# Optimization experiments

Hardware: AMD Instinct MI355X
Metric: run time of the kernel (lower is better)

The kernel has to match this reference:

```python
import jax, jax.numpy as jnp
from jax import lax
import numpy as np

H = W = 768
N_BOXES = 512
C1, C2 = 32, 64
POOL = 5
NUM_CLASSES = 4
BN_EPS = 1e-5


def setup_inputs() -> dict:
    key = jax.random.key(0)
    ks = jax.random.split(key, 20)
    image = jax.random.normal(ks[0], (1, 3, H, W), jnp.float32)
    # valid boxes: xmax>xmin, ymax>ymin, inside [0, W)
    xmin = jax.random.randint(ks[1], (N_BOXES,), 0, W - 256)
    ymin = jax.random.randint(ks[2], (N_BOXES,), 0, H - 256)
    bw = jax.random.randint(ks[3], (N_BOXES,), 8, 256)
    bh = jax.random.randint(ks[4], (N_BOXES,), 8, 256)
    boxes = jnp.stack([xmin, ymin, xmin + bw, ymin + bh], axis=1).astype(jnp.int32)
    conv1_w = jax.random.normal(ks[5], (C1, 3, 3, 3), jnp.float32) * 0.1
    conv1_b = jax.random.normal(ks[6], (C1,), jnp.float32) * 0.01
    bn1_g = 1.0 + 0.1 * jax.random.normal(ks[7], (C1,), jnp.float32)
    bn1_b = 0.1 * jax.random.normal(ks[8], (C1,), jnp.float32)
    bn1_m = 0.1 * jax.random.normal(ks[9], (C1,), jnp.float32)
    bn1_v = jax.random.uniform(ks[10], (C1,), jnp.float32, 0.5, 1.5)
    conv2_w = jax.random.normal(ks[11], (C2, C1, 3, 3), jnp.float32) * 0.05
    conv2_b = jax.random.normal(ks[12], (C2,), jnp.float32) * 0.01
    bn2_g = 1.0 + 0.1 * jax.random.normal(ks[13], (C2,), jnp.float32)
    bn2_b = 0.1 * jax.random.normal(ks[14], (C2,), jnp.float32)
    bn2_m = 0.1 * jax.random.normal(ks[15], (C2,), jnp.float32)
    bn2_v = jax.random.uniform(ks[16], (C2,), jnp.float32, 0.5, 1.5)
    fc1_w = jax.random.normal(ks[17], (128, C2 * POOL * POOL), jnp.float32) * 0.02
    fc1_b = jnp.zeros((128,), jnp.float32)
    fc2_w = jax.random.normal(ks[18], (NUM_CLASSES, 128), jnp.float32) * 0.05
    fc2_b = jnp.zeros((NUM_CLASSES,), jnp.float32)
    return dict(image=image, boxes=boxes,
                conv1_w=conv1_w, conv1_b=conv1_b, bn1_g=bn1_g, bn1_b=bn1_b, bn1_m=bn1_m, bn1_v=bn1_v,
                conv2_w=conv2_w, conv2_b=conv2_b, bn2_g=bn2_g, bn2_b=bn2_b, bn2_m=bn2_m, bn2_v=bn2_v,
                fc1_w=fc1_w, fc1_b=fc1_b, fc2_w=fc2_w, fc2_b=fc2_b)


def _conv(x, w, b):
    y = lax.conv_general_dilated(x, w, (1, 1), ((1, 1), (1, 1)),
                                 dimension_numbers=("NCHW", "OIHW", "NCHW"))
    return y + b[None, :, None, None]


def _bn(x, g, b, m, v):
    scale = g / jnp.sqrt(v + BN_EPS)
    return x * scale[None, :, None, None] + (b - m * scale)[None, :, None, None]


def _forward(image, boxes, conv1_w, conv1_b, bn1_g, bn1_b, bn1_m, bn1_v,
             conv2_w, conv2_b, bn2_g, bn2_b, bn2_m, bn2_v,
             fc1_w, fc1_b, fc2_w, fc2_b):
    # backbone: Conv -> ReLU -> BN (order as in source), twice
    x = _bn(jax.nn.relu(_conv(image, conv1_w, conv1_b)), bn1_g, bn1_b, bn1_m, bn1_v)
    x = _bn(jax.nn.relu(_conv(x, conv2_w, conv2_b)), bn2_g, bn2_b, bn2_m, bn2_v)
    feat = x[0]  # [C2, H, W], batch assumed 1 as in the per-box slicing loop
    # integral image for exact adaptive-avg-pool over integer index rectangles
    integ = jnp.pad(feat, ((0, 0), (1, 0), (1, 0))).cumsum(1).cumsum(2)  # [C2,H+1,W+1]
    xmin, ymin, xmax, ymax = boxes[:, 0], boxes[:, 1], boxes[:, 2], boxes[:, 3]
    bh = ymax - ymin
    bw = xmax - xmin
    i = jnp.arange(POOL)
    # AdaptiveAvgPool2d bin edges: start=floor(i*L/5), end=ceil((i+1)*L/5)
    y0 = ymin[:, None] + (i * bh[:, None]) // POOL            # [N,5]
    y1 = ymin[:, None] + ((i + 1) * bh[:, None] + POOL - 1) // POOL
    x0 = xmin[:, None] + (i * bw[:, None]) // POOL
    x1 = xmin[:, None] + ((i + 1) * bw[:, None] + POOL - 1) // POOL

    def rect(ys, xs):  # [C2, N, 5, 5]
        return integ[:, ys[:, :, None], xs[:, None, :]]

    s = rect(y1, x1) - rect(y0, x1) - rect(y1, x0) + rect(y0, x0)
    area = ((y1 - y0)[:, :, None] * (x1 - x0)[:, None, :]).astype(feat.dtype)  # [N,5,5]
    pooled = s / area[None]                                    # [C2,N,5,5]
    flat = pooled.transpose(1, 0, 2, 3).reshape(boxes.shape[0], -1)  # [N, C2*25]
    h1 = jax.nn.relu(flat @ fc1_w.T + fc1_b)  # dropout is identity in eval
    return h1 @ fc2_w.T + fc2_b               # [N, num_classes]


def reference(image, boxes, conv1_w, conv1_b, bn1_g, bn1_b, bn1_m, bn1_v,
              conv2_w, conv2_b, bn2_g, bn2_b, bn2_m, bn2_v,
              fc1_w, fc1_b, fc2_w, fc2_b):
    return _forward(image, boxes, conv1_w, conv1_b, bn1_g, bn1_b, bn1_m, bn1_v,
                    conv2_w, conv2_b, bn2_g, bn2_b, bn2_m, bn2_v,
                    fc1_w, fc1_b, fc2_w, fc2_b)
```

## Files before the change

### kernel.cpp

```cpp
#include <hip/hip_runtime.h>
#include <hip/hip_bf16.h>

#define HH 768
#define WW 768
#define HWSZ (HH*WW)
#define BN_EPS 1e-5f
#define SEG 8
#define NSEG 96

typedef __attribute__((ext_vector_type(8))) short bf16x8;
typedef __attribute__((ext_vector_type(4))) float f32x4;

__device__ __forceinline__ float bf2f(unsigned short u) {
  union { unsigned int i; float f; } v; v.i = ((unsigned int)u) << 16; return v.f;
}
__device__ __forceinline__ unsigned short f2bf(float f) {
  union { float f; unsigned int i; } v; v.f = f;
  unsigned int x = v.i;
  return (unsigned short)((x + 0x7fffu + ((x >> 16) & 1u)) >> 16);
}
__device__ __forceinline__ float ldf(const void* p, int i, int flag) {
  return flag ? bf2f(((const unsigned short*)p)[i]) : ((const float*)p)[i];
}

#define DPP_ADD(v, CTRL) do {                                              \
    union { float f; int i; } _u; _u.f = (v);                              \
    int _t = __builtin_amdgcn_update_dpp(0, _u.i, (CTRL), 0xf, 0xf, true); \
    union { int i; float f; } _w; _w.i = _t;                               \
    (v) += _w.f;                                                           \
  } while (0)
__device__ __forceinline__ float row_prefix16(float v) {
  DPP_ADD(v, 0x111);
  DPP_ADD(v, 0x112);
  DPP_ADD(v, 0x114);
  DPP_ADD(v, 0x118);
  return v;
}

__device__ __forceinline__ int detect_flag(const void* v1) {
  const unsigned short* v1raw = (const unsigned short*)v1;
  int ok = 1;
  #pragma unroll
  for (int j = 0; j < 4; ++j) {
    unsigned short u = v1raw[2*j];
    if (u < 0x3E00u || u > 0x4040u) ok = 0;
  }
  return ok;
}

__global__ void k_prep(const void* __restrict__ c1b,
                       const void* __restrict__ g1, const void* __restrict__ b1,
                       const void* __restrict__ m1, const void* __restrict__ v1,
                       const void* __restrict__ c2b, const void* __restrict__ g2,
                       const void* __restrict__ b2, const void* __restrict__ m2,
                       const void* __restrict__ v2, const void* __restrict__ w1,
                       const void* __restrict__ fb1, const void* __restrict__ fw2,
                       const void* __restrict__ fb2, const void* __restrict__ w2,
                       const void* __restrict__ fw1,
                       int* __restrict__ flagp, float* __restrict__ cst,
                       unsigned short* __restrict__ A2, unsigned short* __restrict__ A1,
                       unsigned short* __restrict__ w1c)
{
  int flag = detect_flag(v1);
  int tid = threadIdx.x, bid = blockIdx.x;
  int gid = bid * 256 + tid;

  if (bid == 0) {
    if (tid == 0) *flagp = flag;
    float* bias1 = cst + 864;
    float* sc1   = cst + 896;
    float* sh1   = cst + 928;
    float* bias2 = cst + 960;
    float* sc2   = cst + 1024;
    float* sh2   = cst + 1088;
    float* fb1c  = cst + 1152;
    float* w2c   = cst + 1280;
    float* fb2c  = cst + 1792;
    if (tid < 32) {
      float s = ldf(g1, tid, flag) * rsqrtf(ldf(v1, tid, flag) + BN_EPS);
      sc1[tid] = s;
      sh1[tid] = ldf(b1, tid, flag) - ldf(m1, tid, flag) * s;
      bias1[tid] = ldf(c1b, tid, flag);
    }
    if (tid < 64) {
      float s = ldf(g2, tid, flag) * rsqrtf(ldf(v2, tid, flag) + BN_EPS);
      sc2[tid] = s;
      sh2[tid] = ldf(b2, tid, flag) - ldf(m2, tid, flag) * s;
      bias2[tid] = ldf(c2b, tid, flag);
    }
    if (tid < 128) fb1c[tid] = ldf(fb1, tid, flag);
    if (tid < 4)   fb2c[tid] = ldf(fb2, tid, flag);
    for (int i = tid; i < 512; i += 256) w2c[i] = ldf(fw2, i, flag);
  }
  if (gid < 80*288) {
    int o = gid / 288, k = gid % 288, tap = k >> 5, ci = k & 31;
    A2[gid] = (o < 64) ? f2bf(ldf(w2, (o*32 + ci)*9 + tap, flag)) : (unsigned short)0;
  }
  if (gid < 32*64) {
    int o = gid >> 6, k = gid & 63, tap = k >> 2, ci = k & 3;
    A1[gid] = (tap < 9 && ci < 3) ? f2bf(ldf(w1, o*27 + ci*9 + tap, flag))
                                  : (unsigned short)0;
  }
  for (int i = gid; i < 128*1600; i += 128*256) {
    int t = i / 1600, r = i % 1600, cell = r >> 6, c = r & 63;
    w1c[i] = f2bf(ldf(fw1, t*1600 + c*25 + cell, flag));
  }
}

__global__ __launch_bounds__(256) void k_conv1m(const void* __restrict__ img,
    const int* __restrict__ flagp, const unsigned short* __restrict__ A1,
    const float* __restrict__ cst, unsigned short* __restrict__ feat1)
{
  const float* bias1 = cst + 864;
  const float* sc1   = cst + 896;
  const float* sh1   = cst + 928;
  int flag = *flagp;
  __shared__ unsigned short tile[18 * 34 * 4];
  int tid = threadIdx.x;
  int x0 = blockIdx.x * 32, ybase = blockIdx.y * 16;

  for (int idx = tid; idx < 18*34; idx += 256) {
    int r = idx / 34, p = idx % 34;
    int gy = ybase - 1 + r, gx = x0 - 1 + p;
    unsigned short e0 = 0, e1 = 0, e2 = 0;
    if (gy >= 0 && gy < HH && gx >= 0 && gx < WW) {
      e0 = f2bf(ldf(img, 0*HWSZ + gy*WW + gx, flag));
      e1 = f2bf(ldf(img, 1*HWSZ + gy*WW + gx, flag));
      e2 = f2bf(ldf(img, 2*HWSZ + gy*WW + gx, flag));
    }
    ushort4 pk; pk.x = e0; pk.y = e1; pk.z = e2; pk.w = 0;
    *(ushort4*)(tile + idx*4) = pk;
  }

  int w = tid >> 6, lane = tid & 63, quad = lane >> 4, l16 = lane & 15;
  bf16x8 a1f[2][2];
  #pragma unroll
  for (int mt = 0; mt < 2; ++mt)
    #pragma unroll
    for (int kt = 0; kt < 2; ++kt)
      a1f[mt][kt] = *(const bf16x8*)(A1 + (mt*16 + l16)*64 + kt*32 + quad*8);
  int t0 = 2*quad, t1 = 2*quad + 1;
  int ky0 = t0/3, kx0 = t0%3, ky1 = t1/3, kx1 = t1%3;
  __syncthreads();

  for (int dyw = 0; dyw < 4; ++dyw) {
    int dy = dyw*4 + w;
    int y = ybase + dy;
    f32x4 acc[2][2];
    #pragma unroll
    for (int mt = 0; mt < 2; ++mt)
      #pragma unroll
      for (int i = 0; i < 2; ++i)
        acc[mt][i] = (f32x4){0.f,0.f,0.f,0.f};
    #pragma unroll
    for (int i = 0; i < 2; ++i) {
      int pxb = i*16 + l16;
      union { uint2 u[2]; bf16x8 v; } b0;
      b0.u[0] = *(const uint2*)(tile + ((dy + ky0)*34 + pxb + kx0)*4);
      b0.u[1] = *(const uint2*)(tile + ((dy + ky1)*34 + pxb + kx1)*4);
      union { uint2 u[2]; bf16x8 v; } b1v;
      b1v.u[0] = *(const uint2*)(tile + ((dy + 2)*34 + pxb + 2)*4);
      b1v.u[1] = make_uint2(0u, 0u);
      #pragma unroll
      for (int mt = 0; mt < 2; ++mt) {
        acc[mt][i] = __builtin_amdgcn_mfma_f32_16x16x32_bf16(a1f[mt][0], b0.v, acc[mt][i], 0, 0, 0);
        acc[mt][i] = __builtin_amdgcn_mfma_f32_16x16x32_bf16(a1f[mt][1], b1v.v, acc[mt][i], 0, 0, 0);
      }
    }
    #pragma unroll
    for (int mt = 0; mt < 2; ++mt) {
      int cb = mt*16 + quad*4;
      float bs0 = bias1[cb], bs1 = bias1[cb+1], bs2 = bias1[cb+2], bs3 = bias1[cb+3];
      float s0 = sc1[cb], s1 = sc1[cb+1], s2 = sc1[cb+2], s3 = sc1[cb+3];
      float h0 = sh1[cb], h1 = sh1[cb+1], h2 = sh1[cb+2], h3 = sh1[cb+3];
      #pragma unroll
      for (int i = 0; i < 2; ++i) {
        int px = x0 + i*16 + l16;
        ushort4 pk;
        pk.x = f2bf(fmaxf(acc[mt][i][0] + bs0, 0.f) * s0 + h0);
        pk.y = f2bf(fmaxf(acc[mt][i][1] + bs1, 0.f) * s1 + h1);
        pk.z = f2bf(fmaxf(acc[mt][i][2] + bs2, 0.f) * s2 + h2);
        pk.w = f2bf(fmaxf(acc[mt][i][3] + bs3, 0.f) * s3 + h3);
        *(ushort4*)(feat1 + ((size_t)(y*WW + px))*32 + cb) = pk;
      }
    }
  }
}

__global__ __launch_bounds__(256) void k_conv2t(const unsigned short* __restrict__ feat1,
    const unsigned short* __restrict__ A2, const float* __restrict__ cst,
    float* __restrict__ T)
{
  const float* bias2 = cst + 960;
  const float* sc2   = cst + 1024;
  const float* sh2   = cst + 1088;
  __shared__ unsigned short tile[10 * 34 * 40];
  int tid = threadIdx.x;
  int xb = blockIdx.x, ys = blockIdx.y;
  int x0 = xb * 32, ybase = ys * SEG;

  for (int idx = tid; idx < 10*34*4; idx += 256) {
    int q = idx & 3, p = (idx >> 2) % 34, r = idx / 136;
    int gy = ybase - 1 + r, gx = x0 - 1 + p;
    uint4 val = make_uint4(0u, 0u, 0u, 0u);
    if (gy >= 0 && gy < HH && gx >= 0 && gx < WW)
      val = *(const uint4*)(feat1 + (gy*WW + gx)*32 + q*8);
    *(uint4*)(tile + (r*34 + p)*40 + q*8) = val;
  }

  int w = tid >> 6, lane = tid & 63, quad = lane >> 4, l16 = lane & 15;
  int m = w * 16 + l16;
  bf16x8 afrag[9];
  #pragma unroll
  for (int t = 0; t < 9; ++t)
    afrag[t] = *(const bf16x8*)(A2 + m*288 + t*32 + quad*8);
  float bs[4], scv[4], shv[4];
  #pragma unroll
  for (int r = 0; r < 4; ++r) {
    int c = w*16 + quad*4 + r;
    bs[r] = bias2[c]; scv[r] = sc2[c]; shv[r] = sh2[c];
  }
  __syncthreads();

  f32x4 ys0 = (f32x4){0.f,0.f,0.f,0.f};
  f32x4 ys1 = (f32x4){0.f,0.f,0.f,0.f};
  int cbase = w*16 + quad*4;
  for (int dy = 0; dy < SEG; ++dy) {
    int y = ybase + dy;
    f32x4 acc[2];
    acc[0] = (f32x4){0.f,0.f,0.f,0.f};
    acc[1] = (f32x4){0.f,0.f,0.f,0.f};
    #pragma unroll
    for (int t = 0; t < 9; ++t) {
      int ky = t / 3, kx = t % 3;
      #pragma unroll
      for (int i = 0; i < 2; ++i) {
        int px = i*16 + l16 + kx;
        bf16x8 b = *(const bf16x8*)(tile + ((dy + ky)*34 + px)*40 + quad*8);
        acc[i] = __builtin_amdgcn_mfma_f32_16x16x32_bf16(afrag[t], b, acc[i], 0, 0, 0);
      }
    }
    #pragma unroll
    for (int r = 0; r < 4; ++r) {
      float v0 = fmaxf(acc[0][r] + bs[r], 0.f) * scv[r] + shv[r];
      float v1 = fmaxf(acc[1][r] + bs[r], 0.f) * scv[r] + shv[r];
      v0 = row_prefix16(v0);
      v1 = row_prefix16(v1);
      v1 += __shfl(v0, 15, 16);
      ys0[r] += v0;
      ys1[r] += v1;
    }
    *(f32x4*)(T + ((size_t)(y*WW + x0 + l16))*64 + cbase)      = ys0;
    *(f32x4*)(T + ((size_t)(y*WW + x0 + 16 + l16))*64 + cbase) = ys1;
  }
}

__global__ __launch_bounds__(256) void k_cgen(const float* __restrict__ T,
                                              float* __restrict__ C)
{
  __shared__ float Sp[NSEG*24];
  int cc = blockIdx.x, tid = threadIdx.x;
  for (int idx = tid; idx < NSEG*24; idx += 256) {
    int i = idx / 24, j = idx % 24;
    Sp[idx] = T[((size_t)((i*SEG + SEG-1)*WW + j*32 + 31))*64 + cc];
  }
  __syncthreads();
  if (tid < 24) {
    float run = 0.f;
    for (int i = 0; i < NSEG; ++i) { run += Sp[i*24 + tid]; Sp[i*24 + tid] = run; }
  }
  __syncthreads();
  if (tid < NSEG) {
    float run = 0.f;
    #pragma unroll
    for (int j = 0; j < 24; ++j) { run += Sp[tid*24 + j]; Sp[tid*24 + j] = run; }
  }
  __syncthreads();
  for (int idx = tid; idx < NSEG*24; idx += 256)
    C[((size_t)idx)*64 + cc] = Sp[idx];
}

__global__ __launch_bounds__(256) void k_ab(const float* __restrict__ T,
    const float* __restrict__ C, float* __restrict__ A, float* __restrict__ Bp)
{
  int part = blockIdx.y, tid = threadIdx.x;
  int c = tid & 63, s = tid >> 6;
  if (part == 0) {
    int y = blockIdx.x * 4 + s;
    float run = 0.f;
    #pragma unroll
    for (int j = 0; j < 24; ++j) {
      run += T[((size_t)(y*WW + j*32 + 31))*64 + c];
      A[((size_t)(y*24 + j))*64 + c] = run;
    }
  } else {
    int x = blockIdx.x * 4 + s;
    int j = x >> 5;
    float run = 0.f;
    #pragma unroll 4
    for (int i = 0; i < NSEG; ++i) {
      run += T[((size_t)((i*SEG + SEG-1)*WW + x))*64 + c];
      float cj = (j > 0) ? C[((size_t)(i*24 + (j-1)))*64 + c] : 0.f;
      Bp[((size_t)(i*WW + x))*64 + c] = run + cj;
    }
  }
}

__device__ __forceinline__ float icorner(const float* __restrict__ T,
    const float* __restrict__ A, const float* __restrict__ Bp,
    int c, int yy, int xx)
{
  int i = yy >> 3, j = xx >> 5;
  float v = T[((size_t)(yy*WW + xx))*64 + c];
  if (j > 0) v += A[((size_t)(yy*24 + (j-1)))*64 + c];
  if (i > 0) v += Bp[((size_t)((i-1)*WW + xx))*64 + c];
  return v;
}

__global__ __launch_bounds__(256) void k_roi3(const float* __restrict__ T,
    const float* __restrict__ A, const float* __restrict__ Bp,
    const int* __restrict__ boxes, unsigned short* __restrict__ flat)
{
  int b = blockIdx.x;
  int xmin = boxes[b*4 + 0], ymin = boxes[b*4 + 1];
  int xmax = boxes[b*4 + 2], ymax = boxes[b*4 + 3];
  int bh = ymax - ymin, bw = xmax - xmin;
  for (int idx = threadIdx.x; idx < 1600; idx += 256) {
    int c = idx & 63, cell = idx >> 6, i = cell / 5, j = cell % 5;
    int y0 = ymin + (i*bh)/5,  y1 = ymin + ((i+1)*bh + 4)/5;
    int x0 = xmin + (j*bw)/5,  x1 = xmin + ((j+1)*bw + 4)/5;
    float s = icorner(T, A, Bp, c, y1-1, x1-1);
    if (y0 > 0)           s -= icorner(T, A, Bp, c, y0-1, x1-1);
    if (x0 > 0)           s -= icorner(T, A, Bp, c, y1-1, x0-1);
    if (y0 > 0 && x0 > 0) s += icorner(T, A, Bp, c, y0-1, x0-1);
    float area = (float)((y1 - y0) * (x1 - x0));
    flat[b*1600 + cell*64 + c] = f2bf(s / area);
  }
}

__global__ __launch_bounds__(256) void k_fcm(const unsigned short* __restrict__ flat,
    const unsigned short* __restrict__ w1c, const float* __restrict__ cst,
    const int* __restrict__ flagp, void* __restrict__ out)
{
  const float* fb1c = cst + 1152;
  const float* w2c  = cst + 1280;
  const float* fb2c = cst + 1792;
  __shared__ unsigned short sflat[16 * 1608];
  __shared__ float hbuf[16 * 132];
  int tid = threadIdx.x;
  int b0 = blockIdx.x * 16;
  for (int ii = tid; ii < 3200; ii += 256) {
    int bi = ii / 200, ch = ii % 200;
    *(uint4*)(sflat + bi*1608 + ch*8) = *(const uint4*)(flat + (b0 + bi)*1600 + ch*8);
  }
  __syncthreads();
  int w = tid >> 6, lane = tid & 63, quad = lane >> 4, l16 = lane & 15;
  f32x4 acc[2];
  acc[0] = (f32x4){0.f,0.f,0.f,0.f};
  acc[1] = (f32x4){0.f,0.f,0.f,0.f};
  for (int kt = 0; kt < 50; ++kt) {
    bf16x8 b = *(const bf16x8*)(sflat + l16*1608 + kt*32 + quad*8);
    #pragma unroll
    for (int mt = 0; mt < 2; ++mt) {
      bf16x8 a = *(const bf16x8*)(w1c + ((w*2 + mt)*16 + l16)*1600 + kt*32 + quad*8);
      acc[mt] = __builtin_amdgcn_mfma_f32_16x16x32_bf16(a, b, acc[mt], 0, 0, 0);
    }
  }
  #pragma unroll
  for (int mt = 0; mt < 2; ++mt) {
    #pragma unroll
    for (int r = 0; r < 4; ++r) {
      int h = (w*2 + mt)*16 + quad*4 + r;
      hbuf[l16*132 + h] = fmaxf(acc[mt][r] + fb1c[h], 0.f);
    }
  }
  __syncthreads();
  if (tid < 64) {
    int bi = tid >> 2, o = tid & 3;
    float a2 = fb2c[o];
    for (int k = 0; k < 128; ++k) a2 += hbuf[bi*132 + k] * w2c[o*128 + k];
    if (*flagp) ((unsigned short*)out)[(b0 + bi)*4 + o] = f2bf(a2);
    else        ((float*)out)[(b0 + bi)*4 + o] = a2;
  }
}

__global__ __launch_bounds__(256) void k_conv2_c16(const unsigned short* __restrict__ feat1,
    const unsigned short* __restrict__ A2, const float* __restrict__ cst,
    float* __restrict__ chunk, int c0, int cnw)
{
  const float* bias2 = cst + 960;
  const float* sc2   = cst + 1024;
  const float* sh2   = cst + 1088;
  __shared__ unsigned short tile[3 * 130 * 40];
  int tid = threadIdx.x;
  int y = blockIdx.y, x0 = blockIdx.x * 128;
  for (int idx = tid; idx < 3*130*4; idx += 256) {
    int q = idx & 3, p = (idx >> 2) % 130, r = idx / 520;
    int gy = y - 1 + r, gx = x0 - 1 + p;
    uint4 val = make_uint4(0u, 0u, 0u, 0u);
    if (gy >= 0 && gy < HH && gx >= 0 && gx < WW)
      val = *(const uint4*)(feat1 + (gy*WW + gx)*32 + q*8);
    *(uint4*)(tile + (r*130 + p)*40 + q*8) = val;
  }
  __syncthreads();
  int w = tid >> 6, lane = tid & 63, quad = lane >> 4, l16 = lane & 15;
  int m = c0 + l16;
  f32x4 acc[2];
  acc[0] = (f32x4){0.f,0.f,0.f,0.f};
  acc[1] = (f32x4){0.f,0.f,0.f,0.f};
  #pragma unroll
  for (int t = 0; t < 9; ++t) {
    int ky = t / 3, kx = t % 3;
    bf16x8 a = *(const bf16x8*)(A2 + m*288 + t*32 + quad*8);
    #pragma unroll
    for (int i = 0; i < 2; ++i) {
      int px = w*32 + i*16 + l16 + kx;
      bf16x8 b = *(const bf16x8*)(tile + (ky*130 + px)*40 + quad*8);
      acc[i] = __builtin_amdgcn_mfma_f32_16x16x32_bf16(a, b, acc[i], 0, 0, 0);
    }
  }
  #pragma unroll
  for (int r = 0; r < 4; ++r) {
    int cl = quad*4 + r;
    if (cl < cnw) {
      int c = c0 + cl;
      float bsv = bias2[c], s = sc2[c], sh = sh2[c];
      float* dst = chunk + cl*HWSZ + y*WW;
      #pragma unroll
      for (int i = 0; i < 2; ++i) {
        float v = fmaxf(acc[i][r] + bsv, 0.f) * s + sh;
        dst[x0 + w*32 + i*16 + l16] = v;
      }
    }
  }
}
__global__ __launch_bounds__(256) void k_csy(float* __restrict__ buf) {
  int t = blockIdx.x * 256 + threadIdx.x;
  int c = t / WW, x = t % WW;
  float* p = buf + c*HWSZ + x;
  float run = 0.f;
  for (int yb = 0; yb < HH; yb += 16) {
    float v[16];
    #pragma unroll
    for (int j = 0; j < 16; ++j) v[j] = p[(yb + j) * WW];
    #pragma unroll
    for (int j = 0; j < 16; ++j) { run += v[j]; v[j] = run; }
    #pragma unroll
    for (int j = 0; j < 16; ++j) p[(yb + j) * WW] = v[j];
  }
}
__global__ __launch_bounds__(256) void k_csx(float* __restrict__ buf) {
  int row = blockIdx.x * 4 + (threadIdx.x >> 6);
  int lane = threadIdx.x & 63;
  float* p = buf + (long)row * WW;
  float carry = 0.f;
  for (int ch = 0; ch < 12; ++ch) {
    float v = p[ch*64 + lane];
    #pragma unroll
    for (int off = 1; off < 64; off <<= 1) {
      float t = __shfl_up(v, off);
      v = (lane >= off) ? v + t : v;
    }
    v += carry;
    p[ch*64 + lane] = v;
    carry = __shfl(v, 63);
  }
}
__global__ __launch_bounds__(256) void k_roi(const float* __restrict__ integ,
    const int* __restrict__ boxes, unsigned short* __restrict__ flat, int c0, int cn)
{
  int b = blockIdx.x;
  int xmin = boxes[b*4 + 0], ymin = boxes[b*4 + 1];
  int xmax = boxes[b*4 + 2], ymax = boxes[b*4 + 3];
  int bh = ymax - ymin, bw = xmax - xmin;
  for (int idx = threadIdx.x; idx < cn*25; idx += 256) {
    int cl = idx / 25, cell = idx % 25, i = cell / 5, j = cell % 5;
    int y0 = ymin + (i*bh)/5,      y1 = ymin + ((i+1)*bh + 4)/5;
    int x0 = xmin + (j*bw)/5,      x1 = xmin + ((j+1)*bw + 4)/5;
    const float* I = integ + cl*HWSZ;
    float a  = I[(y1-1)*WW + (x1-1)];
    float bl = (y0 > 0) ? I[(y0-1)*WW + (x1-1)] : 0.f;
    float cr = (x0 > 0) ? I[(y1-1)*WW + (x0-1)] : 0.f;
    float d  = (y0 > 0 && x0 > 0) ? I[(y0-1)*WW + (x0-1)] : 0.f;
    float s = a - bl - cr + d;
    float area = (float)((y1 - y0) * (x1 - x0));
    flat[b*1600 + cell*64 + (c0 + cl)] = f2bf(s / area);
  }
}

extern "C" void kernel_launch(void* const* d_in, const int* in_sizes, int n_in,
                              void* d_out, int out_size, void* d_ws, size_t ws_size,
                              hipStream_t stream) {
  const void* img = d_in[0];
  const int* boxes = (const int*)d_in[1];
  const void* c1w = d_in[2];  const void* c1b = d_in[3];
  const void* g1  = d_in[4];  const void* b1  = d_in[5];
  const void* m1  = d_in[6];  const void* v1  = d_in[7];
  const void* c2w = d_in[8];  const void* c2b = d_in[9];
  const void* g2  = d_in[10]; const void* b2  = d_in[11];
  const void* m2  = d_in[12]; const void* v2  = d_in[13];
  const void* fw1 = d_in[14]; const void* fb1 = d_in[15];
  const void* fw2 = d_in[16]; const void* fb2 = d_in[17];

  char* ws = (char*)d_ws;
  unsigned short* A2 = (unsigned short*)ws;
  unsigned short* A1 = (unsigned short*)(ws + 46080);
  float* cst = (float*)(ws + 50176);
  int* flag = (int*)(ws + 57360);
  unsigned short* w1c  = (unsigned short*)(ws + 3592224);
  unsigned short* flat = (unsigned short*)(ws + 4001824);
  unsigned short* feat1 = (unsigned short*)(ws + 7278624);
  float* T = (float*)(ws + 45027360);
  float* Aarr = (float*)(ws + 7278624);
  float* Bparr = Aarr + (size_t)768*24*64;
  float* Carr = Bparr + (size_t)NSEG*768*64;

  const size_t base = 45027360;
  int cn;
  if      (ws_size >= base + 64ull*HWSZ*4) cn = 64;
  else if (ws_size >= base + 16ull*HWSZ*4) cn = 16;
  else if (ws_size >= base +  8ull*HWSZ*4) cn = 8;
  else if (ws_size >= base +  4ull*HWSZ*4) cn = 4;
  else if (ws_size >= base +  2ull*HWSZ*4) cn = 2;
  else                                     cn = 1;

  hipLaunchKernelGGL(k_prep, dim3(128), dim3(256), 0, stream,
                     c1b, g1, b1, m1, v1, c2b, g2, b2, m2, v2, c1w,
                     fb1, fw2, fb2, c2w, fw1, flag, cst, A2, A1, w1c);
  hipLaunchKernelGGL(k_conv1m, dim3(24, 48), dim3(256), 0, stream,
                     img, flag, A1, cst, feat1);

  if (cn == 64) {
    hipLaunchKernelGGL(k_conv2t, dim3(24, NSEG), dim3(256), 0, stream,
                       feat1, A2, cst, T);
    hipLaunchKernelGGL(k_cgen, dim3(64), dim3(256), 0, stream, T, Carr);
    hipLaunchKernelGGL(k_ab, dim3(192, 2), dim3(256), 0, stream, T, Carr, Aarr, Bparr);
    hipLaunchKernelGGL(k_roi3, dim3(512), dim3(256), 0, stream,
                       T, Aarr, Bparr, boxes, flat);
  } else {
    for (int c0 = 0; c0 < 64; c0 += cn) {
      hipLaunchKernelGGL(k_conv2_c16, dim3(6, 768), dim3(256), 0, stream,
                         feat1, A2, cst, T, c0, cn);
      hipLaunchKernelGGL(k_csy, dim3(cn*3), dim3(256), 0, stream, T);
      hipLaunchKernelGGL(k_csx, dim3(cn*192), dim3(256), 0, stream, T);
      hipLaunchKernelGGL(k_roi, dim3(512), dim3(256), 0, stream, T, boxes, flat, c0, cn);
    }
  }
  hipLaunchKernelGGL(k_fcm, dim3(32), dim3(256), 0, stream, flat, w1c, cst, flag,
                     d_out);
}
```

Baseline: 228.0 us.

## Fuse conv1 into conv2 tile kernel and parallelize row/column prefix scans

Conv1 is now computed per block on a 10x34 halo tile straight from the image into shared memory, and conv2 reads that tile directly. This removes the feat1 round trip through global memory and one kernel launch. The cost is recomputing conv1 on overlapping halo rows and columns, plus more shared memory per block. Separately, k_ab splits each row and column scan across four thread groups and combines partial sums through shared memory, which gives four times more blocks.

```diff
diff --git a/kernel.cpp b/kernel.cpp
--- a/kernel.cpp
+++ b/kernel.cpp
@@ -107,21 +107,27 @@
   }
 }
 
-__global__ __launch_bounds__(256) void k_conv1m(const void* __restrict__ img,
+__global__ __launch_bounds__(256) void k_conv12t(const void* __restrict__ img,
     const int* __restrict__ flagp, const unsigned short* __restrict__ A1,
-    const float* __restrict__ cst, unsigned short* __restrict__ feat1)
+    const unsigned short* __restrict__ A2, const float* __restrict__ cst,
+    float* __restrict__ T)
 {
   const float* bias1 = cst + 864;
   const float* sc1   = cst + 896;
   const float* sh1   = cst + 928;
+  const float* bias2 = cst + 960;
+  const float* sc2   = cst + 1024;
+  const float* sh2   = cst + 1088;
+  __shared__ unsigned short ftile[10 * 34 * 40];
+  __shared__ unsigned short itile[12 * 36 * 4];
   int flag = *flagp;
-  __shared__ unsigned short tile[18 * 34 * 4];
   int tid = threadIdx.x;
-  int x0 = blockIdx.x * 32, ybase = blockIdx.y * 16;
-
-  for (int idx = tid; idx < 18*34; idx += 256) {
-    int r = idx / 34, p = idx % 34;
-    int gy = ybase - 1 + r, gx = x0 - 1 + p;
+  int xb = blockIdx.x, ys = blockIdx.y;
+  int x0 = xb * 32, ybase = ys * SEG;
+
+  for (int idx = tid; idx < 12*36; idx += 256) {
+    int r = idx / 36, p = idx % 36;
+    int gy = ybase - 2 + r, gx = x0 - 2 + p;
     unsigned short e0 = 0, e1 = 0, e2 = 0;
     if (gy >= 0 && gy < HH && gx >= 0 && gx < WW) {
       e0 = f2bf(ldf(img, 0*HWSZ + gy*WW + gx, flag));
@@ -129,10 +135,11 @@
       e2 = f2bf(ldf(img, 2*HWSZ + gy*WW + gx, flag));
     }
     ushort4 pk; pk.x = e0; pk.y = e1; pk.z = e2; pk.w = 0;
-    *(ushort4*)(tile + idx*4) = pk;
+    *(ushort4*)(itile + idx*4) = pk;
   }
 
   int w = tid >> 6, lane = tid & 63, quad = lane >> 4, l16 = lane & 15;
+
   bf16x8 a1f[2][2];
   #pragma unroll
   for (int mt = 0; mt < 2; ++mt)
@@ -141,74 +148,7 @@
       a1f[mt][kt] = *(const bf16x8*)(A1 + (mt*16 + l16)*64 + kt*32 + quad*8);
   int t0 = 2*quad, t1 = 2*quad + 1;
   int ky0 = t0/3, kx0 = t0%3, ky1 = t1/3, kx1 = t1%3;
-  __syncthreads();
-
-  for (int dyw = 0; dyw < 4; ++dyw) {
-    int dy = dyw*4 + w;
-    int y = ybase + dy;
-    f32x4 acc[2][2];
-    #pragma unroll
-    for (int mt = 0; mt < 2; ++mt)
-      #pragma unroll
-      for (int i = 0; i < 2; ++i)
-        acc[mt][i] = (f32x4){0.f,0.f,0.f,0.f};
-    #pragma unroll
-    for (int i = 0; i < 2; ++i) {
-      int pxb = i*16 + l16;
-      union { uint2 u[2]; bf16x8 v; } b0;
-      b0.u[0] = *(const uint2*)(tile + ((dy + ky0)*34 + pxb + kx0)*4);
-      b0.u[1] = *(const uint2*)(tile + ((dy + ky1)*34 + pxb + kx1)*4);
-      union { uint2 u[2]; bf16x8 v; } b1v;
-      b1v.u[0] = *(const uint2*)(tile + ((dy + 2)*34 + pxb + 2)*4);
-      b1v.u[1] = make_uint2(0u, 0u);
-      #pragma unroll
-      for (int mt = 0; mt < 2; ++mt) {
-        acc[mt][i] = __builtin_amdgcn_mfma_f32_16x16x32_bf16(a1f[mt][0], b0.v, acc[mt][i], 0, 0, 0);
-        acc[mt][i] = __builtin_amdgcn_mfma_f32_16x16x32_bf16(a1f[mt][1], b1v.v, acc[mt][i], 0, 0, 0);
-      }
-    }
-    #pragma unroll
-    for (int mt = 0; mt < 2; ++mt) {
-      int cb = mt*16 + quad*4;
-      float bs0 = bias1[cb], bs1 = bias1[cb+1], bs2 = bias1[cb+2], bs3 = bias1[cb+3];
-      float s0 = sc1[cb], s1 = sc1[cb+1], s2 = sc1[cb+2], s3 = sc1[cb+3];
-      float h0 = sh1[cb], h1 = sh1[cb+1], h2 = sh1[cb+2], h3 = sh1[cb+3];
-      #pragma unroll
-      for (int i = 0; i < 2; ++i) {
-        int px = x0 + i*16 + l16;
-        ushort4 pk;
-        pk.x = f2bf(fmaxf(acc[mt][i][0] + bs0, 0.f) * s0 + h0);
-        pk.y = f2bf(fmaxf(acc[mt][i][1] + bs1, 0.f) * s1 + h1);
-        pk.z = f2bf(fmaxf(acc[mt][i][2] + bs2, 0.f) * s2 + h2);
-        pk.w = f2bf(fmaxf(acc[mt][i][3] + bs3, 0.f) * s3 + h3);
-        *(ushort4*)(feat1 + ((size_t)(y*WW + px))*32 + cb) = pk;
-      }
-    }
-  }
-}
-
-__global__ __launch_bounds__(256) void k_conv2t(const unsigned short* __restrict__ feat1,
-    const unsigned short* __restrict__ A2, const float* __restrict__ cst,
-    float* __restrict__ T)
-{
-  const float* bias2 = cst + 960;
-  const float* sc2   = cst + 1024;
-  const float* sh2   = cst + 1088;
-  __shared__ unsigned short tile[10 * 34 * 40];
-  int tid = threadIdx.x;
-  int xb = blockIdx.x, ys = blockIdx.y;
-  int x0 = xb * 32, ybase = ys * SEG;
-
-  for (int idx = tid; idx < 10*34*4; idx += 256) {
-    int q = idx & 3, p = (idx >> 2) % 34, r = idx / 136;
-    int gy = ybase - 1 + r, gx = x0 - 1 + p;
-    uint4 val = make_uint4(0u, 0u, 0u, 0u);
-    if (gy >= 0 && gy < HH && gx >= 0 && gx < WW)
-      val = *(const uint4*)(feat1 + (gy*WW + gx)*32 + q*8);
-    *(uint4*)(tile + (r*34 + p)*40 + q*8) = val;
-  }
-
-  int w = tid >> 6, lane = tid & 63, quad = lane >> 4, l16 = lane & 15;
+
   int m = w * 16 + l16;
   bf16x8 afrag[9];
   #pragma unroll
@@ -219,6 +159,45 @@
   for (int r = 0; r < 4; ++r) {
     int c = w*16 + quad*4 + r;
     bs[r] = bias2[c]; scv[r] = sc2[c]; shv[r] = sh2[c];
+  }
+  __syncthreads();
+
+  for (int u = w; u < 30; u += 4) {
+    int r = u / 3, nt = u % 3;
+    int pxb = nt*16 + l16;
+    int pp = (pxb <= 33) ? pxb : 33;
+    union { uint2 q[2]; bf16x8 v; } b0;
+    b0.q[0] = *(const uint2*)(itile + ((r + ky0)*36 + pp + kx0)*4);
+    b0.q[1] = *(const uint2*)(itile + ((r + ky1)*36 + pp + kx1)*4);
+    union { uint2 q[2]; bf16x8 v; } b1v;
+    b1v.q[0] = *(const uint2*)(itile + ((r + 2)*36 + pp + 2)*4);
+    b1v.q[1] = make_uint2(0u, 0u);
+    f32x4 acc[2];
+    acc[0] = (f32x4){0.f,0.f,0.f,0.f};
+    acc[1] = (f32x4){0.f,0.f,0.f,0.f};
+    #pragma unroll
+    for (int mt = 0; mt < 2; ++mt) {
+      acc[mt] = __builtin_amdgcn_mfma_f32_16x16x32_bf16(a1f[mt][0], b0.v, acc[mt], 0, 0, 0);
+      acc[mt] = __builtin_amdgcn_mfma_f32_16x16x32_bf16(a1f[mt][1], b1v.v, acc[mt], 0, 0, 0);
+    }
+    int py = ybase - 1 + r, gx = x0 - 1 + pxb;
+    int inside = (py >= 0 && py < HH && gx >= 0 && gx < WW);
+    if (pxb < 34) {
+      #pragma unroll
+      for (int mt = 0; mt < 2; ++mt) {
+        int cb = mt*16 + quad*4;
+        ushort4 pk;
+        if (inside) {
+          pk.x = f2bf(fmaxf(acc[mt][0] + bias1[cb+0], 0.f) * sc1[cb+0] + sh1[cb+0]);
+          pk.y = f2bf(fmaxf(acc[mt][1] + bias1[cb+1], 0.f) * sc1[cb+1] + sh1[cb+1]);
+          pk.z = f2bf(fmaxf(acc[mt][2] + bias1[cb+2], 0.f) * sc1[cb+2] + sh1[cb+2]);
+          pk.w = f2bf(fmaxf(acc[mt][3] + bias1[cb+3], 0.f) * sc1[cb+3] + sh1[cb+3]);
+        } else {
+          pk.x = pk.y = pk.z = pk.w = 0;
+        }
+        *(ushort4*)(ftile + (r*34 + pxb)*40 + cb) = pk;
+      }
+    }
   }
   __syncthreads();
 
@@ -236,7 +215,7 @@
       #pragma unroll
       for (int i = 0; i < 2; ++i) {
         int px = i*16 + l16 + kx;
-        bf16x8 b = *(const bf16x8*)(tile + ((dy + ky)*34 + px)*40 + quad*8);
+        bf16x8 b = *(const bf16x8*)(ftile + ((dy + ky)*34 + px)*40 + quad*8);
         acc[i] = __builtin_amdgcn_mfma_f32_16x16x32_bf16(afrag[t], b, acc[i], 0, 0, 0);
       }
     }
@@ -283,25 +262,46 @@
 __global__ __launch_bounds__(256) void k_ab(const float* __restrict__ T,
     const float* __restrict__ C, float* __restrict__ A, float* __restrict__ Bp)
 {
+  __shared__ float gtot[4][64];
   int part = blockIdx.y, tid = threadIdx.x;
-  int c = tid & 63, s = tid >> 6;
+  int c = tid & 63, g = tid >> 6;
   if (part == 0) {
-    int y = blockIdx.x * 4 + s;
+    int y = blockIdx.x;
+    float vals[6];
     float run = 0.f;
     #pragma unroll
-    for (int j = 0; j < 24; ++j) {
+    for (int jj = 0; jj < 6; ++jj) {
+      int j = g*6 + jj;
       run += T[((size_t)(y*WW + j*32 + 31))*64 + c];
-      A[((size_t)(y*24 + j))*64 + c] = run;
-    }
+      vals[jj] = run;
+    }
+    gtot[g][c] = run;
+    __syncthreads();
+    float off = 0.f;
+    for (int gg = 0; gg < g; ++gg) off += gtot[gg][c];
+    #pragma unroll
+    for (int jj = 0; jj < 6; ++jj)
+      A[((size_t)(y*24 + g*6 + jj))*64 + c] = vals[jj] + off;
   } else {
-    int x = blockIdx.x * 4 + s;
+    int x = blockIdx.x;
     int j = x >> 5;
+    float vals[24];
     float run = 0.f;
     #pragma unroll 4
-    for (int i = 0; i < NSEG; ++i) {
+    for (int ii = 0; ii < 24; ++ii) {
+      int i = g*24 + ii;
       run += T[((size_t)((i*SEG + SEG-1)*WW + x))*64 + c];
+      vals[ii] = run;
+    }
+    gtot[g][c] = run;
+    __syncthreads();
+    float off = 0.f;
+    for (int gg = 0; gg < g; ++gg) off += gtot[gg][c];
+    #pragma unroll 4
+    for (int ii = 0; ii < 24; ++ii) {
+      int i = g*24 + ii;
       float cj = (j > 0) ? C[((size_t)(i*24 + (j-1)))*64 + c] : 0.f;
-      Bp[((size_t)(i*WW + x))*64 + c] = run + cj;
+      Bp[((size_t)(i*WW + x))*64 + c] = vals[ii] + off + cj;
     }
   }
 }
@@ -384,6 +384,79 @@
   }
 }
 
+__global__ __launch_bounds__(256) void k_conv1m(const void* __restrict__ img,
+    const int* __restrict__ flagp, const unsigned short* __restrict__ A1,
+    const float* __restrict__ cst, unsigned short* __restrict__ feat1)
+{
+  const float* bias1 = cst + 864;
+  const float* sc1   = cst + 896;
+  const float* sh1   = cst + 928;
+  int flag = *flagp;
+  __shared__ unsigned short tile[18 * 34 * 4];
+  int tid = threadIdx.x;
+  int x0 = blockIdx.x * 32, ybase = blockIdx.y * 16;
+  for (int idx = tid; idx < 18*34; idx += 256) {
+    int r = idx / 34, p = idx % 34;
+    int gy = ybase - 1 + r, gx = x0 - 1 + p;
+    unsigned short e0 = 0, e1 = 0, e2 = 0;
+    if (gy >= 0 && gy < HH && gx >= 0 && gx < WW) {
+      e0 = f2bf(ldf(img, 0*HWSZ + gy*WW + gx, flag));
+      e1 = f2bf(ldf(img, 1*HWSZ + gy*WW + gx, flag));
+      e2 = f2bf(ldf(img, 2*HWSZ + gy*WW + gx, flag));
+    }
+    ushort4 pk; pk.x = e0; pk.y = e1; pk.z = e2; pk.w = 0;
+    *(ushort4*)(tile + idx*4) = pk;
+  }
+  int w = tid >> 6, lane = tid & 63, quad = lane >> 4, l16 = lane & 15;
+  bf16x8 a1f[2][2];
+  #pragma unroll
+  for (int mt = 0; mt < 2; ++mt)
+    #pragma unroll
+    for (int kt = 0; kt < 2; ++kt)
+      a1f[mt][kt] = *(const bf16x8*)(A1 + (mt*16 + l16)*64 + kt*32 + quad*8);
+  int t0 = 2*quad, t1 = 2*quad + 1;
+  int ky0 = t0/3, kx0 = t0%3, ky1 = t1/3, kx1 = t1%3;
+  __syncthreads();
+  for (int dyw = 0; dyw < 4; ++dyw) {
+    int dy = dyw*4 + w;
+    int y = ybase + dy;
+    f32x4 acc[2][2];
+    #pragma unroll
+    for (int mt = 0; mt < 2; ++mt)
+      #pragma unroll
+      for (int i = 0; i < 2; ++i)
+        acc[mt][i] = (f32x4){0.f,0.f,0.f,0.f};
+    #pragma unroll
+    for (int i = 0; i < 2; ++i) {
+      int pxb = i*16 + l16;
+      union { uint2 q[2]; bf16x8 v; } b0;
+      b0.q[0] = *(const uint2*)(tile + ((dy + ky0)*34 + pxb + kx0)*4);
+      b0.q[1] = *(const uint2*)(tile + ((dy + ky1)*34 + pxb + kx1)*4);
+      union { uint2 q[2]; bf16x8 v; } b1v;
+      b1v.q[0] = *(const uint2*)(tile + ((dy + 2)*34 + pxb + 2)*4);
+      b1v.q[1] = make_uint2(0u, 0u);
+      #pragma unroll
+      for (int mt = 0; mt < 2; ++mt) {
+        acc[mt][i] = __builtin_amdgcn_mfma_f32_16x16x32_bf16(a1f[mt][0], b0.v, acc[mt][i], 0, 0, 0);
+        acc[mt][i] = __builtin_amdgcn_mfma_f32_16x16x32_bf16(a1f[mt][1], b1v.v, acc[mt][i], 0, 0, 0);
+      }
+    }
+    #pragma unroll
+    for (int mt = 0; mt < 2; ++mt) {
+      int cb = mt*16 + quad*4;
+      #pragma unroll
+      for (int i = 0; i < 2; ++i) {
+        int px = x0 + i*16 + l16;
+        ushort4 pk;
+        pk.x = f2bf(fmaxf(acc[mt][i][0] + bias1[cb+0], 0.f) * sc1[cb+0] + sh1[cb+0]);
+        pk.y = f2bf(fmaxf(acc[mt][i][1] + bias1[cb+1], 0.f) * sc1[cb+1] + sh1[cb+1]);
+        pk.z = f2bf(fmaxf(acc[mt][i][2] + bias1[cb+2], 0.f) * sc1[cb+2] + sh1[cb+2]);
+        pk.w = f2bf(fmaxf(acc[mt][i][3] + bias1[cb+3], 0.f) * sc1[cb+3] + sh1[cb+3]);
+        *(ushort4*)(feat1 + ((size_t)(y*WW + px))*32 + cb) = pk;
+      }
+    }
+  }
+}
 __global__ __launch_bounds__(256) void k_conv2_c16(const unsigned short* __restrict__ feat1,
     const unsigned short* __restrict__ A2, const float* __restrict__ cst,
     float* __restrict__ chunk, int c0, int cnw)
@@ -527,17 +600,17 @@
   hipLaunchKernelGGL(k_prep, dim3(128), dim3(256), 0, stream,
                      c1b, g1, b1, m1, v1, c2b, g2, b2, m2, v2, c1w,
                      fb1, fw2, fb2, c2w, fw1, flag, cst, A2, A1, w1c);
-  hipLaunchKernelGGL(k_conv1m, dim3(24, 48), dim3(256), 0, stream,
-                     img, flag, A1, cst, feat1);
 
   if (cn == 64) {
-    hipLaunchKernelGGL(k_conv2t, dim3(24, NSEG), dim3(256), 0, stream,
-                       feat1, A2, cst, T);
+    hipLaunchKernelGGL(k_conv12t, dim3(24, NSEG), dim3(256), 0, stream,
+                       img, flag, A1, A2, cst, T);
     hipLaunchKernelGGL(k_cgen, dim3(64), dim3(256), 0, stream, T, Carr);
-    hipLaunchKernelGGL(k_ab, dim3(192, 2), dim3(256), 0, stream, T, Carr, Aarr, Bparr);
+    hipLaunchKernelGGL(k_ab, dim3(768, 2), dim3(256), 0, stream, T, Carr, Aarr, Bparr);
     hipLaunchKernelGGL(k_roi3, dim3(512), dim3(256), 0, stream,
                        T, Aarr, Bparr, boxes, flat);
   } else {
+    hipLaunchKernelGGL(k_conv1m, dim3(24, 48), dim3(256), 0, stream,
+                       img, flag, A1, cst, feat1);
     for (int c0 = 0; c0 < 64; c0 += cn) {
       hipLaunchKernelGGL(k_conv2_c16, dim3(6, 768), dim3(256), 0, stream,
                          feat1, A2, cst, T, c0, cn);
```

Measured after the change: 210.2 us. -7.8%, faster.
